# Kernel optimization log

Hardware: AMD Instinct MI355X
Metric: run time of the kernel (lower is better)

The kernel has to match this reference:

```python
import jax, jax.numpy as jnp
import numpy as np

HEADERS = 8
LN_EPS = 1e-3  # keras LayerNormalization default


def setup_inputs() -> dict:
    key = jax.random.key(0)
    ks = jax.random.split(key, 8)
    B, H, W, C = 16, 48, 160, 512
    shi = C // HEADERS
    scale = 1.0 / np.sqrt(C)
    return {
        "x": jax.random.normal(ks[0], (B, H, W, C), dtype=jnp.float32),
        "w_mask": jax.random.normal(ks[1], (shi,), dtype=jnp.float32) * (1.0 / np.sqrt(shi)),
        "b_mask": jnp.zeros((1,), dtype=jnp.float32),
        "w1": jax.random.normal(ks[2], (C, C), dtype=jnp.float32) * scale,
        "b1": jnp.zeros((C,), dtype=jnp.float32),
        "gamma": jnp.ones((C,), dtype=jnp.float32),
        "beta": jnp.zeros((C,), dtype=jnp.float32),
        "w2": jax.random.normal(ks[3], (C, C), dtype=jnp.float32) * scale,
        "b2": jnp.zeros((C,), dtype=jnp.float32),
    }


def reference(x, w_mask, b_mask, w1, b1, gamma, beta, w2, b2):
    B, H, W, C = x.shape
    g = HEADERS
    shi = C // g
    # split channels into headers: [B, g, H*W, shi]
    xh = x.reshape(B, H, W, g, shi).transpose(0, 3, 1, 2, 4).reshape(B, g, H * W, shi)
    # 1x1 conv to single channel -> attention logits over spatial positions
    logits = jnp.einsum('bgnc,c->bgn', xh, w_mask) + b_mask[0]
    # att_scale=True and headers>1 -> rescale
    logits = logits / jnp.sqrt(jnp.asarray(shi, x.dtype))
    attn = jax.nn.softmax(logits, axis=-1)  # softmax over H*W
    # single-query attention pooling per header -> [B, g, shi] -> [B, C]
    ctx = jnp.einsum('bgnc,bgn->bgc', xh, attn).reshape(B, C)
    # transform: 1x1 conv -> LayerNorm over C -> ReLU -> 1x1 conv
    h = ctx @ w1 + b1
    mu = jnp.mean(h, axis=-1, keepdims=True)
    var = jnp.mean(jnp.square(h - mu), axis=-1, keepdims=True)
    hn = (h - mu) * jax.lax.rsqrt(var + LN_EPS) * gamma + beta
    t = jax.nn.relu(hn) @ w2 + b2  # [B, C]
    return x + t[:, None, None, :]
```

## Files before the change

### kernel.cpp

```cpp
#include <hip/hip_runtime.h>
#include <math.h>

#define Bb 16
#define Hh 48
#define Ww 160
#define Cc 512
#define Gg 8
#define SHI 64
#define Nn (Hh * Ww)
#define NCHUNK 16
#define CHUNK (Nn / NCHUNK)
#define LN_EPS 1e-3f

__device__ __forceinline__ float wave_sum(float v) {
#pragma unroll
    for (int o = 32; o > 0; o >>= 1) v += __shfl_xor(v, o);
    return v;
}
__device__ __forceinline__ float wave_max(float v) {
#pragma unroll
    for (int o = 32; o > 0; o >>= 1) v = fmaxf(v, __shfl_xor(v, o));
    return v;
}

__global__ __launch_bounds__(256) void k_logits(const float* __restrict__ x,
                                                const float* __restrict__ w_mask,
                                                const float* __restrict__ b_mask,
                                                float* __restrict__ logits) {
    int wave = (blockIdx.x * 256 + threadIdx.x) >> 6;
    int lane = threadIdx.x & 63;
    if (wave >= Bb * Nn) return;
    const float* xp = x + (size_t)wave * Cc + lane * 8;
    float4 a0 = *(const float4*)(xp);
    float4 a1 = *(const float4*)(xp + 4);
    int cw = (lane & 7) * 8;
    float4 m0 = *(const float4*)(w_mask + cw);
    float4 m1 = *(const float4*)(w_mask + cw + 4);
    float s = a0.x * m0.x + a0.y * m0.y + a0.z * m0.z + a0.w * m0.w
            + a1.x * m1.x + a1.y * m1.y + a1.z * m1.z + a1.w * m1.w;
    s += __shfl_xor(s, 1);
    s += __shfl_xor(s, 2);
    s += __shfl_xor(s, 4);
    if ((lane & 7) == 0) {
        int g = lane >> 3;
        int b = wave / Nn;
        int n = wave - b * Nn;
        logits[((size_t)b * Gg + g) * Nn + n] = (s + b_mask[0]) * 0.125f;
    }
}

__global__ __launch_bounds__(256) void k_softmax(const float* __restrict__ logits,
                                                 float* __restrict__ attn) {
    int row = blockIdx.x;
    const float* lp = logits + (size_t)row * Nn;
    float* ap = attn + (size_t)row * Nn;
    int t = threadIdx.x, lane = t & 63, wid = t >> 6;
    __shared__ float red[4];

    float m = -1e30f;
    for (int i = t; i < Nn; i += 256) m = fmaxf(m, lp[i]);
    m = wave_max(m);
    if (lane == 0) red[wid] = m;
    __syncthreads();
    float M = fmaxf(fmaxf(red[0], red[1]), fmaxf(red[2], red[3]));
    __syncthreads();

    float s = 0.f;
    for (int i = t; i < Nn; i += 256) {
        float e = __expf(lp[i] - M);
        ap[i] = e;
        s += e;
    }
    s = wave_sum(s);
    if (lane == 0) red[wid] = s;
    __syncthreads();
    float inv = 1.0f / (red[0] + red[1] + red[2] + red[3]);
    for (int i = t; i < Nn; i += 256) ap[i] *= inv;
}

__global__ __launch_bounds__(256) void k_ctx(const float* __restrict__ x,
                                             const float* __restrict__ attn,
                                             float* __restrict__ partial) {
    int blk = blockIdx.x;
    int chunk = blk & (NCHUNK - 1);
    int g = (blk >> 4) & 7;
    int b = blk >> 7;
    int t = threadIdx.x;
    int c = t & 63;
    int nb = t >> 6;

    const float* xp = x + (size_t)b * Nn * Cc + (size_t)g * SHI + c;
    const float* ap = attn + ((size_t)b * Gg + g) * Nn;

    float acc = 0.f;
    int n0 = chunk * CHUNK + nb;
    int n1 = chunk * CHUNK + CHUNK;
#pragma unroll 8
    for (int n = n0; n < n1; n += 4) {
        acc += ap[n] * xp[(size_t)n * Cc];
    }

    __shared__ float red[256];
    red[t] = acc;
    __syncthreads();
    if (t < 64) {
        float v = red[t] + red[t + 64] + red[t + 128] + red[t + 192];
        partial[(size_t)chunk * (Bb * Cc) + (size_t)b * Cc + g * SHI + t] = v;
    }
}

__global__ __launch_bounds__(512) void k_mlp(const float* __restrict__ partial,
                                             const float* __restrict__ w1,
                                             const float* __restrict__ b1,
                                             const float* __restrict__ gamma,
                                             const float* __restrict__ beta,
                                             const float* __restrict__ w2,
                                             const float* __restrict__ b2,
                                             float* __restrict__ tvec) {
    int b = blockIdx.x;
    int c = threadIdx.x;
    int lane = c & 63, wid = c >> 6;
    __shared__ float cs[Cc];
    __shared__ float hs[Cc];
    __shared__ float red[8];

    float cv = 0.f;
#pragma unroll
    for (int k = 0; k < NCHUNK; ++k) cv += partial[(size_t)k * (Bb * Cc) + (size_t)b * Cc + c];
    cs[c] = cv;
    __syncthreads();

    float h = b1[c];
#pragma unroll 8
    for (int k = 0; k < Cc; ++k) h = fmaf(cs[k], w1[(size_t)k * Cc + c], h);

    float s = wave_sum(h);
    if (lane == 0) red[wid] = s;
    __syncthreads();
    float mu = 0.f;
#pragma unroll
    for (int k = 0; k < 8; ++k) mu += red[k];
    mu *= (1.0f / Cc);
    __syncthreads();
    float d = h - mu;
    float sq = wave_sum(d * d);
    if (lane == 0) red[wid] = sq;
    __syncthreads();
    float var = 0.f;
#pragma unroll
    for (int k = 0; k < 8; ++k) var += red[k];
    var *= (1.0f / Cc);
    float hn = d * rsqrtf(var + LN_EPS) * gamma[c] + beta[c];
    hs[c] = fmaxf(hn, 0.f);
    __syncthreads();

    float tv = b2[c];
#pragma unroll 8
    for (int k = 0; k < Cc; ++k) tv = fmaf(hs[k], w2[(size_t)k * Cc + c], tv);
    tvec[(size_t)b * Cc + c] = tv;
}

__global__ __launch_bounds__(256) void k_resid(const float4* __restrict__ x4,
                                               const float4* __restrict__ t4,
                                               float4* __restrict__ o4) {
    int b = blockIdx.y;
    int idx = blockIdx.x * 256 + threadIdx.x;
    int c4 = idx & 127;
    size_t off = (size_t)b * (Nn * (Cc / 4)) + idx;
    float4 xv = x4[off];
    float4 tv = t4[b * (Cc / 4) + c4];
    o4[off] = make_float4(xv.x + tv.x, xv.y + tv.y, xv.z + tv.z, xv.w + tv.w);
}

extern "C" void kernel_launch(void* const* d_in, const int* in_sizes, int n_in,
                              void* d_out, int out_size, void* d_ws, size_t ws_size,
                              hipStream_t stream) {
    const float* x      = (const float*)d_in[0];
    const float* w_mask = (const float*)d_in[1];
    const float* b_mask = (const float*)d_in[2];
    const float* w1     = (const float*)d_in[3];
    const float* b1     = (const float*)d_in[4];
    const float* gamma  = (const float*)d_in[5];
    const float* beta   = (const float*)d_in[6];
    const float* w2     = (const float*)d_in[7];
    const float* b2     = (const float*)d_in[8];
    float* out = (float*)d_out;

    float* ws      = (float*)d_ws;
    float* logits  = ws;
    float* attn    = logits + (size_t)Bb * Gg * Nn;
    float* partial = attn + (size_t)Bb * Gg * Nn;
    float* tvec    = partial + (size_t)NCHUNK * Bb * Cc;

    k_logits<<<(Bb * Nn) / 4, 256, 0, stream>>>(x, w_mask, b_mask, logits);
    k_softmax<<<Bb * Gg, 256, 0, stream>>>(logits, attn);
    k_ctx<<<Bb * Gg * NCHUNK, 256, 0, stream>>>(x, attn, partial);
    k_mlp<<<Bb, Cc, 0, stream>>>(partial, w1, b1, gamma, beta, w2, b2, tvec);
    k_resid<<<dim3((Nn * Cc / 4) / 256, Bb), 256, 0, stream>>>(
        (const float4*)x, (const float4*)tvec, (float4*)out);
}
```

Measured before the change: 580.7 us.

## Fuse logits, softmax and context pooling into one online-softmax pass over x

Replaces the separate logits, softmax and context kernels with one kernel that reads x once per chunk. It computes logits per position and keeps a running max, sum and weighted context in flash-attention style, then writes per-chunk partials with their max and sum. The MLP kernel merges the chunks by rescaling them against the global max before the transform. This removes a second full read of x and the logits/attn round trips through workspace. The residual kernel now handles two float4s per thread with nontemporal loads and stores. The cost is extra exp work per position and a larger number of partials for k_mlp to combine.

```diff
diff --git a/kernel.cpp b/kernel.cpp
--- a/kernel.cpp
+++ b/kernel.cpp
@@ -8,9 +8,11 @@
 #define Gg 8
 #define SHI 64
 #define Nn (Hh * Ww)
-#define NCHUNK 16
-#define CHUNK (Nn / NCHUNK)
+#define NCH 64
+#define POSCH (Nn / NCH)
 #define LN_EPS 1e-3f
+
+typedef float v4f __attribute__((ext_vector_type(4)));
 
 __device__ __forceinline__ float wave_sum(float v) {
 #pragma unroll
@@ -23,93 +25,75 @@
     return v;
 }
 
-__global__ __launch_bounds__(256) void k_logits(const float* __restrict__ x,
-                                                const float* __restrict__ w_mask,
-                                                const float* __restrict__ b_mask,
-                                                float* __restrict__ logits) {
-    int wave = (blockIdx.x * 256 + threadIdx.x) >> 6;
-    int lane = threadIdx.x & 63;
-    if (wave >= Bb * Nn) return;
-    const float* xp = x + (size_t)wave * Cc + lane * 8;
-    float4 a0 = *(const float4*)(xp);
-    float4 a1 = *(const float4*)(xp + 4);
+__global__ __launch_bounds__(256) void k_pool(const float* __restrict__ x,
+                                              const float* __restrict__ w_mask,
+                                              const float* __restrict__ b_mask,
+                                              float* __restrict__ pctx,
+                                              float* __restrict__ pms) {
+    int chunk = blockIdx.x;
+    int b = blockIdx.y;
+    int t = threadIdx.x;
+    int w = t >> 6;
+    int lane = t & 63;
+    int g = lane >> 3;
+
     int cw = (lane & 7) * 8;
     float4 m0 = *(const float4*)(w_mask + cw);
     float4 m1 = *(const float4*)(w_mask + cw + 4);
-    float s = a0.x * m0.x + a0.y * m0.y + a0.z * m0.z + a0.w * m0.w
-            + a1.x * m1.x + a1.y * m1.y + a1.z * m1.z + a1.w * m1.w;
-    s += __shfl_xor(s, 1);
-    s += __shfl_xor(s, 2);
-    s += __shfl_xor(s, 4);
-    if ((lane & 7) == 0) {
-        int g = lane >> 3;
-        int b = wave / Nn;
-        int n = wave - b * Nn;
-        logits[((size_t)b * Gg + g) * Nn + n] = (s + b_mask[0]) * 0.125f;
-    }
-}
-
-__global__ __launch_bounds__(256) void k_softmax(const float* __restrict__ logits,
-                                                 float* __restrict__ attn) {
-    int row = blockIdx.x;
-    const float* lp = logits + (size_t)row * Nn;
-    float* ap = attn + (size_t)row * Nn;
-    int t = threadIdx.x, lane = t & 63, wid = t >> 6;
-    __shared__ float red[4];
-
-    float m = -1e30f;
-    for (int i = t; i < Nn; i += 256) m = fmaxf(m, lp[i]);
-    m = wave_max(m);
-    if (lane == 0) red[wid] = m;
-    __syncthreads();
-    float M = fmaxf(fmaxf(red[0], red[1]), fmaxf(red[2], red[3]));
-    __syncthreads();
-
-    float s = 0.f;
-    for (int i = t; i < Nn; i += 256) {
-        float e = __expf(lp[i] - M);
-        ap[i] = e;
-        s += e;
-    }
-    s = wave_sum(s);
-    if (lane == 0) red[wid] = s;
-    __syncthreads();
-    float inv = 1.0f / (red[0] + red[1] + red[2] + red[3]);
-    for (int i = t; i < Nn; i += 256) ap[i] *= inv;
-}
-
-__global__ __launch_bounds__(256) void k_ctx(const float* __restrict__ x,
-                                             const float* __restrict__ attn,
-                                             float* __restrict__ partial) {
-    int blk = blockIdx.x;
-    int chunk = blk & (NCHUNK - 1);
-    int g = (blk >> 4) & 7;
-    int b = blk >> 7;
-    int t = threadIdx.x;
-    int c = t & 63;
-    int nb = t >> 6;
-
-    const float* xp = x + (size_t)b * Nn * Cc + (size_t)g * SHI + c;
-    const float* ap = attn + ((size_t)b * Gg + g) * Nn;
-
-    float acc = 0.f;
-    int n0 = chunk * CHUNK + nb;
-    int n1 = chunk * CHUNK + CHUNK;
-#pragma unroll 8
-    for (int n = n0; n < n1; n += 4) {
-        acc += ap[n] * xp[(size_t)n * Cc];
-    }
-
-    __shared__ float red[256];
-    red[t] = acc;
-    __syncthreads();
-    if (t < 64) {
-        float v = red[t] + red[t + 64] + red[t + 128] + red[t + 192];
-        partial[(size_t)chunk * (Bb * Cc) + (size_t)b * Cc + g * SHI + t] = v;
-    }
-}
-
-__global__ __launch_bounds__(512) void k_mlp(const float* __restrict__ partial,
+    float bm = b_mask[0];
+
+    float mrun = -1e30f, srun = 0.f;
+    float acc[8];
+#pragma unroll
+    for (int j = 0; j < 8; ++j) acc[j] = 0.f;
+
+    const float* xbase = x + ((size_t)b * Nn + (size_t)chunk * POSCH) * Cc + lane * 8;
+
+    for (int p = w; p < POSCH; p += 4) {
+        const float* xp = xbase + (size_t)p * Cc;
+        float4 a0 = *(const float4*)(xp);
+        float4 a1 = *(const float4*)(xp + 4);
+        float v[8] = {a0.x, a0.y, a0.z, a0.w, a1.x, a1.y, a1.z, a1.w};
+        float d = a0.x * m0.x + a0.y * m0.y + a0.z * m0.z + a0.w * m0.w
+                + a1.x * m1.x + a1.y * m1.y + a1.z * m1.z + a1.w * m1.w;
+        d += __shfl_xor(d, 1);
+        d += __shfl_xor(d, 2);
+        d += __shfl_xor(d, 4);
+        float l = (d + bm) * 0.125f;
+        float mnew = fmaxf(mrun, l);
+        float scale = __expf(mrun - mnew);
+        float e = __expf(l - mnew);
+        srun = srun * scale + e;
+#pragma unroll
+        for (int j = 0; j < 8; ++j) acc[j] = acc[j] * scale + e * v[j];
+        mrun = mnew;
+    }
+
+    __shared__ float lm[4][8], lsv[4][8];
+    __shared__ float lacc[4][Cc];
+    if ((lane & 7) == 0) { lm[w][g] = mrun; lsv[w][g] = srun; }
+    __syncthreads();
+    float M = fmaxf(fmaxf(lm[0][g], lm[1][g]), fmaxf(lm[2][g], lm[3][g]));
+    float wscale = __expf(mrun - M);
+#pragma unroll
+    for (int j = 0; j < 8; ++j) lacc[w][lane * 8 + j] = acc[j] * wscale;
+    __syncthreads();
+    for (int c = t; c < Cc; c += 256) {
+        float s4 = lacc[0][c] + lacc[1][c] + lacc[2][c] + lacc[3][c];
+        pctx[((size_t)b * NCH + chunk) * Cc + c] = s4;
+    }
+    if (t < 8) {
+        int gg = t;
+        float Mg = fmaxf(fmaxf(lm[0][gg], lm[1][gg]), fmaxf(lm[2][gg], lm[3][gg]));
+        float Sg = lsv[0][gg] * __expf(lm[0][gg] - Mg) + lsv[1][gg] * __expf(lm[1][gg] - Mg)
+                 + lsv[2][gg] * __expf(lm[2][gg] - Mg) + lsv[3][gg] * __expf(lm[3][gg] - Mg);
+        pms[(((size_t)b * Gg + gg) * NCH + chunk) * 2 + 0] = Mg;
+        pms[(((size_t)b * Gg + gg) * NCH + chunk) * 2 + 1] = Sg;
+    }
+}
+
+__global__ __launch_bounds__(512) void k_mlp(const float* __restrict__ pctx,
+                                             const float* __restrict__ pms,
                                              const float* __restrict__ w1,
                                              const float* __restrict__ b1,
                                              const float* __restrict__ gamma,
@@ -118,21 +102,39 @@
                                              const float* __restrict__ b2,
                                              float* __restrict__ tvec) {
     int b = blockIdx.x;
-    int c = threadIdx.x;
-    int lane = c & 63, wid = c >> 6;
+    int t = threadIdx.x;
+    int lane = t & 63, wid = t >> 6;
+    __shared__ float escale[Gg][NCH];
+    __shared__ float Sg[Gg];
     __shared__ float cs[Cc];
     __shared__ float hs[Cc];
     __shared__ float red[8];
 
-    float cv = 0.f;
-#pragma unroll
-    for (int k = 0; k < NCHUNK; ++k) cv += partial[(size_t)k * (Bb * Cc) + (size_t)b * Cc + c];
-    cs[c] = cv;
-    __syncthreads();
-
-    float h = b1[c];
+    {
+        int g = wid, ch = lane;
+        float2 msv = *(const float2*)(pms + (((size_t)b * Gg + g) * NCH + ch) * 2);
+        float M = wave_max(msv.x);
+        float e = __expf(msv.x - M);
+        escale[g][ch] = e;
+        float S = wave_sum(msv.y * e);
+        if (lane == 0) Sg[g] = S;
+    }
+    __syncthreads();
+
+    {
+        int g = t >> 6;
+        float invS = 1.0f / Sg[g];
+        float a = 0.f;
+#pragma unroll 4
+        for (int ch = 0; ch < NCH; ++ch)
+            a += pctx[((size_t)b * NCH + ch) * Cc + t] * escale[g][ch];
+        cs[t] = a * invS;
+    }
+    __syncthreads();
+
+    float h = b1[t];
 #pragma unroll 8
-    for (int k = 0; k < Cc; ++k) h = fmaf(cs[k], w1[(size_t)k * Cc + c], h);
+    for (int k = 0; k < Cc; ++k) h = fmaf(cs[k], w1[(size_t)k * Cc + t], h);
 
     float s = wave_sum(h);
     if (lane == 0) red[wid] = s;
@@ -150,26 +152,31 @@
 #pragma unroll
     for (int k = 0; k < 8; ++k) var += red[k];
     var *= (1.0f / Cc);
-    float hn = d * rsqrtf(var + LN_EPS) * gamma[c] + beta[c];
-    hs[c] = fmaxf(hn, 0.f);
-    __syncthreads();
-
-    float tv = b2[c];
+    float hn = d * rsqrtf(var + LN_EPS) * gamma[t] + beta[t];
+    hs[t] = fmaxf(hn, 0.f);
+    __syncthreads();
+
+    float tv = b2[t];
 #pragma unroll 8
-    for (int k = 0; k < Cc; ++k) tv = fmaf(hs[k], w2[(size_t)k * Cc + c], tv);
-    tvec[(size_t)b * Cc + c] = tv;
-}
-
-__global__ __launch_bounds__(256) void k_resid(const float4* __restrict__ x4,
-                                               const float4* __restrict__ t4,
-                                               float4* __restrict__ o4) {
+    for (int k = 0; k < Cc; ++k) tv = fmaf(hs[k], w2[(size_t)k * Cc + t], tv);
+    tvec[(size_t)b * Cc + t] = tv;
+}
+
+__global__ __launch_bounds__(256) void k_resid(const v4f* __restrict__ x4,
+                                               const v4f* __restrict__ t4,
+                                               v4f* __restrict__ o4) {
     int b = blockIdx.y;
-    int idx = blockIdx.x * 256 + threadIdx.x;
-    int c4 = idx & 127;
+    int idx = (blockIdx.x * 256 + threadIdx.x) * 2;
+    int c4a = idx & 127;
     size_t off = (size_t)b * (Nn * (Cc / 4)) + idx;
-    float4 xv = x4[off];
-    float4 tv = t4[b * (Cc / 4) + c4];
-    o4[off] = make_float4(xv.x + tv.x, xv.y + tv.y, xv.z + tv.z, xv.w + tv.w);
+    v4f xv0 = __builtin_nontemporal_load(&x4[off]);
+    v4f xv1 = __builtin_nontemporal_load(&x4[off + 1]);
+    v4f tv0 = t4[b * (Cc / 4) + c4a];
+    v4f tv1 = t4[b * (Cc / 4) + c4a + 1];
+    v4f o0 = xv0 + tv0;
+    v4f o1 = xv1 + tv1;
+    __builtin_nontemporal_store(o0, &o4[off]);
+    __builtin_nontemporal_store(o1, &o4[off + 1]);
 }
 
 extern "C" void kernel_launch(void* const* d_in, const int* in_sizes, int n_in,
@@ -186,16 +193,13 @@
     const float* b2     = (const float*)d_in[8];
     float* out = (float*)d_out;
 
-    float* ws      = (float*)d_ws;
-    float* logits  = ws;
-    float* attn    = logits + (size_t)Bb * Gg * Nn;
-    float* partial = attn + (size_t)Bb * Gg * Nn;
-    float* tvec    = partial + (size_t)NCHUNK * Bb * Cc;
-
-    k_logits<<<(Bb * Nn) / 4, 256, 0, stream>>>(x, w_mask, b_mask, logits);
-    k_softmax<<<Bb * Gg, 256, 0, stream>>>(logits, attn);
-    k_ctx<<<Bb * Gg * NCHUNK, 256, 0, stream>>>(x, attn, partial);
-    k_mlp<<<Bb, Cc, 0, stream>>>(partial, w1, b1, gamma, beta, w2, b2, tvec);
-    k_resid<<<dim3((Nn * Cc / 4) / 256, Bb), 256, 0, stream>>>(
-        (const float4*)x, (const float4*)tvec, (float4*)out);
-}
+    float* ws   = (float*)d_ws;
+    float* pctx = ws;
+    float* pms  = pctx + (size_t)Bb * NCH * Cc;
+    float* tvec = pms + (size_t)Bb * Gg * NCH * 2;
+
+    k_pool<<<dim3(NCH, Bb), 256, 0, stream>>>(x, w_mask, b_mask, pctx, pms);
+    k_mlp<<<Bb, Cc, 0, stream>>>(pctx, pms, w1, b1, gamma, beta, w2, b2, tvec);
+    k_resid<<<dim3((Nn * Cc / 4) / 512, Bb), 256, 0, stream>>>(
+        (const v4f*)x, (const v4f*)tvec, (v4f*)out);
+}
```

Result: faster. 536.8 us (-7.6%).
